# Kernel tuning notes

Hardware: AMD Instinct MI355X
Metric: run time of the kernel (lower is better)

The kernel has to match this reference:

```python
import jax, jax.numpy as jnp
import numpy as np

DIM = 512
HEADS = 8
HEAD_DIM = DIM // HEADS
SCALE = HEAD_DIM ** -0.5
EPS = 1e-5


def setup_inputs() -> dict:
    key = jax.random.key(0)
    ks = jax.random.split(key, 6)
    B, N, C = 4, 2048, DIM
    x = jax.random.normal(ks[0], (B, N, C), dtype=jnp.float32)
    w_qkv = jax.random.normal(ks[1], (C, 3 * C), dtype=jnp.float32) * (C ** -0.5)
    w_proj = jax.random.normal(ks[2], (C, C), dtype=jnp.float32) * (C ** -0.5)
    b_proj = jax.random.normal(ks[3], (C,), dtype=jnp.float32) * 0.02
    gamma = jnp.ones((C,), dtype=jnp.float32)
    beta = jnp.zeros((C,), dtype=jnp.float32)
    return {"x": x, "w_qkv": w_qkv, "w_proj": w_proj, "b_proj": b_proj,
            "gamma": gamma, "beta": beta}


def reference(x, w_qkv, w_proj, b_proj, gamma, beta):
    B, N, C = x.shape
    # LayerNorm over channel dim
    mu = jnp.mean(x, axis=-1, keepdims=True)
    var = jnp.mean(jnp.square(x - mu), axis=-1, keepdims=True)
    xn = (x - mu) * jax.lax.rsqrt(var + EPS) * gamma + beta
    # QKV projection (fp32, no bias)
    qkv = xn @ w_qkv  # [B, N, 3C]
    qkv = qkv.reshape(B, N, 3, HEADS, HEAD_DIM)
    q = jnp.transpose(qkv[:, :, 0], (0, 2, 1, 3))  # [B, H, N, D]
    k = jnp.transpose(qkv[:, :, 1], (0, 2, 1, 3))
    v = jnp.transpose(qkv[:, :, 2], (0, 2, 1, 3))
    attn = jnp.einsum('bhnd,bhmd->bhnm', q, k) * SCALE
    attn = jax.nn.softmax(attn, axis=-1)
    out = jnp.einsum('bhnm,bhmd->bhnd', attn, v)  # [B, H, N, D]
    out = jnp.transpose(out, (0, 2, 1, 3)).reshape(B, N, C)
    out = out @ w_proj + b_proj
    return x + out
```

## Files before the change

kernel.cpp:

```cpp
#include <hip/hip_runtime.h>
#include <hip/hip_bf16.h>
#include <math.h>

typedef _Float16 f16;
typedef _Float16 half8 __attribute__((ext_vector_type(8)));
typedef _Float16 half4 __attribute__((ext_vector_type(4)));
typedef float f32x4 __attribute__((ext_vector_type(4)));
typedef unsigned int uint;
typedef unsigned int u32x4 __attribute__((ext_vector_type(4)));

#define DIMC 512
#define HEADS 8
#define HD 64
#define BB 4
#define NN 2048
#define MM (BB*NN)
#define NQKV (3*DIMC)
#define SCALE 0.125f
#define LOG2E 1.44269504f
#define EPSLN 1e-5f

__device__ __forceinline__ void g2l16(const void* g, void* l) {
    __builtin_amdgcn_global_load_lds(
        (const __attribute__((address_space(1))) unsigned int*)g,
        (__attribute__((address_space(3))) unsigned int*)l, 16, 0, 0);
}

__device__ __forceinline__ void ln_rows(const float* __restrict__ x,
                                        const float* __restrict__ gamma,
                                        const float* __restrict__ beta,
                                        f16* __restrict__ xn, int blk) {
    int w = threadIdx.x >> 6;
    int lane = threadIdx.x & 63;
    int row = blk * 4 + w;
    const float* xr = x + (size_t)row * DIMC;
    float4 v0 = ((const float4*)xr)[lane * 2];
    float4 v1 = ((const float4*)xr)[lane * 2 + 1];
    float s = v0.x + v0.y + v0.z + v0.w + v1.x + v1.y + v1.z + v1.w;
#pragma unroll
    for (int off = 1; off < 64; off <<= 1) s += __shfl_xor(s, off);
    float mu = s * (1.0f / DIMC);
    float d0 = v0.x - mu, d1 = v0.y - mu, d2 = v0.z - mu, d3 = v0.w - mu;
    float d4 = v1.x - mu, d5 = v1.y - mu, d6 = v1.z - mu, d7 = v1.w - mu;
    float s2 = d0*d0 + d1*d1 + d2*d2 + d3*d3 + d4*d4 + d5*d5 + d6*d6 + d7*d7;
#pragma unroll
    for (int off = 1; off < 64; off <<= 1) s2 += __shfl_xor(s2, off);
    float rstd = rsqrtf(s2 * (1.0f / DIMC) + EPSLN);
    float4 g0 = ((const float4*)gamma)[lane * 2];
    float4 g1 = ((const float4*)gamma)[lane * 2 + 1];
    float4 b0 = ((const float4*)beta)[lane * 2];
    float4 b1 = ((const float4*)beta)[lane * 2 + 1];
    half8 o;
    o[0] = (f16)(d0 * rstd * g0.x + b0.x);
    o[1] = (f16)(d1 * rstd * g0.y + b0.y);
    o[2] = (f16)(d2 * rstd * g0.z + b0.z);
    o[3] = (f16)(d3 * rstd * g0.w + b0.w);
    o[4] = (f16)(d4 * rstd * g1.x + b1.x);
    o[5] = (f16)(d5 * rstd * g1.y + b1.y);
    o[6] = (f16)(d6 * rstd * g1.z + b1.z);
    o[7] = (f16)(d7 * rstd * g1.w + b1.w);
    ((half8*)(xn + (size_t)row * DIMC))[lane] = o;
}

__device__ __forceinline__ void transp_tile(const float* __restrict__ src,
                                            f16* __restrict__ dst,
                                            int R, int C, int k0, int n0) {
    __shared__ f16 t[32][72];
    int tid = threadIdx.x;
    int rr = tid >> 6, col = tid & 63;
#pragma unroll
    for (int p = 0; p < 8; p++) {
        int r = p * 4 + rr;
        t[r][col] = (f16)src[(size_t)(k0 + r) * C + n0 + col];
    }
    __syncthreads();
    int nl = tid >> 2, kc = (tid & 3) * 8;
    half8 v;
#pragma unroll
    for (int j = 0; j < 8; j++) v[j] = t[kc + j][nl];
    *(half8*)&dst[(size_t)(n0 + nl) * R + k0 + kc] = v;
}

__global__ __launch_bounds__(256) void prep_kernel(const float* __restrict__ x,
                                                   const float* __restrict__ gamma,
                                                   const float* __restrict__ beta,
                                                   const float* __restrict__ wqkv,
                                                   const float* __restrict__ wproj,
                                                   f16* __restrict__ xn,
                                                   f16* __restrict__ wqkvt,
                                                   f16* __restrict__ wprojt) {
    int bid = blockIdx.x;
    if (bid < 2048) {
        ln_rows(x, gamma, beta, xn, bid);
    } else if (bid < 2048 + 384) {
        int b2 = bid - 2048;
        int bx = b2 % 24, by = b2 / 24;
        transp_tile(wqkv, wqkvt, DIMC, NQKV, by * 32, bx * 64);
    } else {
        int b2 = bid - 2048 - 384;
        int bx = b2 % 8, by = b2 / 8;
        transp_tile(wproj, wprojt, DIMC, DIMC, by * 32, bx * 64);
    }
}

__device__ __forceinline__ void gemm128_loop(const char* Ag, const char* Bg,
                                             f16* As, f16* Bs, f32x4 (&acc)[4][4]) {
    int tid = threadIdx.x;
    int w = tid >> 6, lane = tid & 63, l15 = lane & 15, quad = lane >> 4;
    int wy = w >> 1, wx = w & 1;
    int off0 = w * 1024 + lane * 16;
    for (int kk = 0; kk < 16; ++kk) {
        __syncthreads();
#pragma unroll
        for (int c = 0; c < 2; ++c) {
            int off = c * 4096 + off0;
            int row = off >> 6, col = off & 63;
            g2l16(Ag + (size_t)row * 1024 + kk * 64 + col, (char*)As + c * 4096 + w * 1024);
            g2l16(Bg + (size_t)row * 1024 + kk * 64 + col, (char*)Bs + c * 4096 + w * 1024);
        }
        __syncthreads();
        half8 af[4], bf[4];
#pragma unroll
        for (int i = 0; i < 4; ++i) {
            af[i] = *(const half8*)((const char*)As + ((wy * 64 + i * 16 + l15) << 6) + quad * 16);
            bf[i] = *(const half8*)((const char*)Bs + ((wx * 64 + i * 16 + l15) << 6) + quad * 16);
        }
#pragma unroll
        for (int i = 0; i < 4; ++i)
#pragma unroll
            for (int j = 0; j < 4; ++j)
                acc[i][j] = __builtin_amdgcn_mfma_f32_16x16x32_f16(af[i], bf[j], acc[i][j], 0, 0, 0);
    }
}

__global__ __launch_bounds__(256) void gemm_qkv(const f16* __restrict__ xn,
                                                const f16* __restrict__ wt,
                                                f16* __restrict__ qb,
                                                f16* __restrict__ kbuf,
                                                f16* __restrict__ vtb) {
    __shared__ __align__(16) f16 As[128 * 32];
    __shared__ __align__(16) f16 Bs[128 * 32];
    int tid = threadIdx.x;
    int w = tid >> 6, lane = tid & 63, l15 = lane & 15, quad = lane >> 4;
    int wy = w >> 1, wx = w & 1;
    int m0 = blockIdx.y * 128, c0 = blockIdx.x * 128;
    f32x4 acc[4][4] = {};
    gemm128_loop((const char*)(xn + (size_t)m0 * DIMC),
                 (const char*)(wt + (size_t)c0 * DIMC), As, Bs, acc);
    int bx = blockIdx.x;
    if (bx < 8) {
        const float QS = SCALE * LOG2E;
        f16* dst = (bx < 4) ? qb : kbuf;
        float mul = (bx < 4) ? QS : 1.0f;
        int cb = (bx < 4) ? c0 : c0 - DIMC;
#pragma unroll
        for (int i = 0; i < 4; ++i)
#pragma unroll
            for (int j = 0; j < 4; ++j)
#pragma unroll
                for (int r = 0; r < 4; ++r) {
                    int m = m0 + wy * 64 + i * 16 + quad * 4 + r;
                    int c = cb + wx * 64 + j * 16 + l15;
                    int b = m >> 11, n = m & 2047;
                    int h = c >> 6, d = c & 63;
                    dst[(((size_t)(b * HEADS + h)) * NN + n) * HD + d] = (f16)(acc[i][j][r] * mul);
                }
    } else {
        __syncthreads();
        f16* T = (f16*)As + w * 512;
        int cb = c0 - 2 * DIMC;
        int dl = lane >> 2, mp = lane & 3;
#pragma unroll
        for (int i = 0; i < 4; ++i)
#pragma unroll
            for (int j = 0; j < 4; ++j) {
                half4 hv;
#pragma unroll
                for (int r = 0; r < 4; ++r) hv[r] = (f16)acc[i][j][r];
                *(half4*)&T[l15 * 20 + quad * 4] = hv;
                half4 rv = *(half4*)&T[dl * 20 + mp * 4];
                int c = cb + wx * 64 + j * 16 + dl;
                int m = m0 + wy * 64 + i * 16 + mp * 4;
                int b = m >> 11, n = m & 2047;
                int h = c >> 6, d = c & 63;
                *(half4*)&vtb[(((size_t)(b * HEADS + h)) * HD + d) * NN + n] = rv;
            }
    }
}

__global__ __launch_bounds__(256, 4) void attn_kernel(const f16* __restrict__ qb,
                                                      const f16* __restrict__ kbuf,
                                                      const f16* __restrict__ vtb,
                                                      f16* __restrict__ ao) {
    __shared__ __align__(16) f16 KV[8192];
    char* Kc = (char*)KV;
    char* Vc = (char*)(KV + 4096);
    int id = blockIdx.x;
    int xcd = id & 7, slot = id >> 3;
    int bh = xcd * 4 + (slot >> 4);
    int qt4 = slot & 15;
    int n0 = qt4 * 128;
    int tid = threadIdx.x, w = tid >> 6, lane = tid & 63, l15 = lane & 15, quad = lane >> 4;
    const f16* Kbase = kbuf + (size_t)bh * NN * HD;
    const f16* Vbase = vtb + (size_t)bh * HD * NN;
    const f16* Qbase = qb + (size_t)bh * NN * HD;
    half8 qf[2][2];
#pragma unroll
    for (int qt = 0; qt < 2; ++qt) {
        const f16* qr = Qbase + (size_t)(n0 + w * 32 + qt * 16 + l15) * HD + quad * 8;
        qf[qt][0] = *(const half8*)qr;
        qf[qt][1] = *(const half8*)(qr + 32);
    }
    f32x4 ot[2][4] = {};
    f32x4 lacc[2] = {};
    half8 ones8;
#pragma unroll
    for (int j = 0; j < 8; ++j) ones8[j] = (f16)1.0f;
    int srow = tid >> 2, part = (tid & 3) * 16;
    int sb = srow * 128, sx = (srow & 7) << 4;
    int scol = part * 2;
    int rx = (l15 & 7) << 4;
    half8 kp0, kp1, vp0, vp1;
    {
        const f16* kg = Kbase + (size_t)srow * HD + part;
        kp0 = ((const half8*)kg)[0]; kp1 = ((const half8*)kg)[1];
        const f16* vg = Vbase + (size_t)srow * NN + part;
        vp0 = ((const half8*)vg)[0]; vp1 = ((const half8*)vg)[1];
    }
    for (int it = 0; it < NN / 64; ++it) {
        __syncthreads();
        *(half8*)(Kc + sb + (scol ^ sx)) = kp0;
        *(half8*)(Kc + sb + ((scol + 16) ^ sx)) = kp1;
        *(half8*)(Vc + sb + (scol ^ sx)) = vp0;
        *(half8*)(Vc + sb + ((scol + 16) ^ sx)) = vp1;
        __syncthreads();
        if (it < NN / 64 - 1) {
            int kt0 = (it + 1) * 64;
            const f16* kg = Kbase + (size_t)(kt0 + srow) * HD + part;
            kp0 = ((const half8*)kg)[0]; kp1 = ((const half8*)kg)[1];
            const f16* vg = Vbase + (size_t)srow * NN + kt0 + part;
            vp0 = ((const half8*)vg)[0]; vp1 = ((const half8*)vg)[1];
        }
        f32x4 s0[4], s1[4];
        __builtin_amdgcn_s_setprio(1);
#pragma unroll
        for (int kt = 0; kt < 4; ++kt) {
            int rb = (kt * 16 + l15) * 128;
            half8 a0 = *(const half8*)(Kc + rb + ((quad * 16) ^ rx));
            half8 a1 = *(const half8*)(Kc + rb + ((64 + quad * 16) ^ rx));
            f32x4 z0 = {};
            z0 = __builtin_amdgcn_mfma_f32_16x16x32_f16(a0, qf[0][0], z0, 0, 0, 0);
            z0 = __builtin_amdgcn_mfma_f32_16x16x32_f16(a1, qf[0][1], z0, 0, 0, 0);
            s0[kt] = z0;
            f32x4 z1 = {};
            z1 = __builtin_amdgcn_mfma_f32_16x16x32_f16(a0, qf[1][0], z1, 0, 0, 0);
            z1 = __builtin_amdgcn_mfma_f32_16x16x32_f16(a1, qf[1][1], z1, 0, 0, 0);
            s1[kt] = z1;
        }
        __builtin_amdgcn_s_setprio(0);
        uint up[2][4][2];
#pragma unroll
        for (int kt = 0; kt < 4; ++kt) {
            up[0][kt][0] = __builtin_bit_cast(uint, __builtin_amdgcn_cvt_pkrtz(
                __builtin_amdgcn_exp2f(s0[kt][0]), __builtin_amdgcn_exp2f(s0[kt][1])));
            up[0][kt][1] = __builtin_bit_cast(uint, __builtin_amdgcn_cvt_pkrtz(
                __builtin_amdgcn_exp2f(s0[kt][2]), __builtin_amdgcn_exp2f(s0[kt][3])));
            up[1][kt][0] = __builtin_bit_cast(uint, __builtin_amdgcn_cvt_pkrtz(
                __builtin_amdgcn_exp2f(s1[kt][0]), __builtin_amdgcn_exp2f(s1[kt][1])));
            up[1][kt][1] = __builtin_bit_cast(uint, __builtin_amdgcn_cvt_pkrtz(
                __builtin_amdgcn_exp2f(s1[kt][2]), __builtin_amdgcn_exp2f(s1[kt][3])));
        }
        __builtin_amdgcn_s_setprio(1);
#pragma unroll
        for (int kc = 0; kc < 2; ++kc) {
            int cb = (kc * 64 + quad * 16) ^ rx;
            half8 av[4];
#pragma unroll
            for (int dt = 0; dt < 4; ++dt)
                av[dt] = *(const half8*)(Vc + (dt * 16 + l15) * 128 + cb);
#pragma unroll
            for (int qt = 0; qt < 2; ++qt) {
                u32x4 pw;
#pragma unroll
                for (int i = 0; i < 2; ++i) {
                    uint x = up[qt][kc * 2][i], y = up[qt][kc * 2 + 1][i];
                    asm volatile("v_permlane32_swap_b32 %0, %1" : "+v"(x), "+v"(y));
                    asm volatile("v_permlane16_swap_b32 %0, %1" : "+v"(x), "+v"(y));
                    pw[i] = x; pw[2 + i] = y;
                }
                half8 pb8 = __builtin_bit_cast(half8, pw);
                lacc[qt] = __builtin_amdgcn_mfma_f32_16x16x32_f16(ones8, pb8, lacc[qt], 0, 0, 0);
#pragma unroll
                for (int dt = 0; dt < 4; ++dt)
                    ot[qt][dt] = __builtin_amdgcn_mfma_f32_16x16x32_f16(av[dt], pb8, ot[qt][dt], 0, 0, 0);
            }
        }
        __builtin_amdgcn_s_setprio(0);
    }
    float inv[2] = { 1.0f / lacc[0][0], 1.0f / lacc[1][0] };
    __syncthreads();
    char* Tc = (char*)(KV + w * 2048);
#pragma unroll
    for (int qt = 0; qt < 2; ++qt)
#pragma unroll
        for (int dt = 0; dt < 4; ++dt) {
            half4 hv;
#pragma unroll
            for (int r = 0; r < 4; ++r) hv[r] = (f16)(ot[qt][dt][r] * inv[qt]);
            *(half4*)(Tc + (qt * 16 + l15) * 128 + ((dt * 32 + quad * 8) ^ rx)) = hv;
        }
    __syncthreads();
    int b = bh >> 3, h = bh & 7;
#pragma unroll
    for (int j = 0; j < 4; ++j) {
        int nl = j * 8 + (lane >> 3);
        int d16 = (lane & 7) * 16;
        half8 v = *(const half8*)(Tc + nl * 128 + (d16 ^ ((nl & 7) << 4)));
        int n = n0 + w * 32 + nl;
        *(half8*)&ao[((size_t)(b * NN + n)) * DIMC + h * HD + (lane & 7) * 8] = v;
    }
}

__global__ __launch_bounds__(256) void gemm_proj(const f16* __restrict__ aob,
                                                 const f16* __restrict__ wt,
                                                 const float* __restrict__ x,
                                                 const float* __restrict__ bias,
                                                 float* __restrict__ out) {
    __shared__ __align__(16) f16 As[128 * 32];
    __shared__ __align__(16) f16 Bs[64 * 32];
    int tid = threadIdx.x;
    int w = tid >> 6, lane = tid & 63, l15 = lane & 15, quad = lane >> 4;
    int m0 = blockIdx.y * 128, c0 = blockIdx.x * 64;
    const char* Ag = (const char*)(aob + (size_t)m0 * DIMC);
    const char* Bg = (const char*)(wt + (size_t)c0 * DIMC);
    f32x4 acc[2][4] = {};
    int off0 = w * 1024 + lane * 16;
    for (int kk = 0; kk < 16; ++kk) {
        __syncthreads();
#pragma unroll
        for (int c = 0; c < 2; ++c) {
            int off = c * 4096 + off0;
            int row = off >> 6, col = off & 63;
            g2l16(Ag + (size_t)row * 1024 + kk * 64 + col, (char*)As + c * 4096 + w * 1024);
        }
        {
            int off = tid * 16;
            int row = off >> 6, col = off & 63;
            g2l16(Bg + (size_t)row * 1024 + kk * 64 + col, (char*)Bs + w * 1024);
        }
        __syncthreads();
        half8 af[2], bf[4];
#pragma unroll
        for (int i = 0; i < 2; ++i)
            af[i] = *(const half8*)((const char*)As + ((w * 32 + i * 16 + l15) << 6) + quad * 16);
#pragma unroll
        for (int j = 0; j < 4; ++j)
            bf[j] = *(const half8*)((const char*)Bs + ((j * 16 + l15) << 6) + quad * 16);
#pragma unroll
        for (int i = 0; i < 2; ++i)
#pragma unroll
            for (int j = 0; j < 4; ++j)
                acc[i][j] = __builtin_amdgcn_mfma_f32_16x16x32_f16(af[i], bf[j], acc[i][j], 0, 0, 0);
    }
#pragma unroll
    for (int i = 0; i < 2; ++i)
#pragma unroll
        for (int j = 0; j < 4; ++j)
#pragma unroll
            for (int r = 0; r < 4; ++r) {
                int m = m0 + w * 32 + i * 16 + quad * 4 + r;
                int c = c0 + j * 16 + l15;
                out[(size_t)m * DIMC + c] = x[(size_t)m * DIMC + c] + bias[c] + acc[i][j][r];
            }
}

extern "C" void kernel_launch(void* const* d_in, const int* in_sizes, int n_in,
                              void* d_out, int out_size, void* d_ws, size_t ws_size,
                              hipStream_t stream) {
    (void)in_sizes; (void)n_in; (void)out_size; (void)ws_size;
    const float* x     = (const float*)d_in[0];
    const float* wqkv  = (const float*)d_in[1];
    const float* wproj = (const float*)d_in[2];
    const float* bproj = (const float*)d_in[3];
    const float* gamma = (const float*)d_in[4];
    const float* beta  = (const float*)d_in[5];
    float* out = (float*)d_out;

    char* ws = (char*)d_ws;
    f16* xn     = (f16*)ws;                 ws += (size_t)MM * DIMC * 2;
    f16* wqkvt  = (f16*)ws;                 ws += (size_t)NQKV * DIMC * 2;
    f16* wprojt = (f16*)ws;                 ws += (size_t)DIMC * DIMC * 2;
    f16* qbuf   = (f16*)ws;                 ws += (size_t)MM * DIMC * 2;
    f16* kbuf   = (f16*)ws;                 ws += (size_t)MM * DIMC * 2;
    f16* vtbuf  = (f16*)ws;                 ws += (size_t)MM * DIMC * 2;
    f16* aobuf  = (f16*)ws;                 ws += (size_t)MM * DIMC * 2;

    prep_kernel<<<2048 + 384 + 128, 256, 0, stream>>>(x, gamma, beta, wqkv, wproj,
                                                      xn, wqkvt, wprojt);
    gemm_qkv<<<dim3(NQKV / 128, MM / 128), 256, 0, stream>>>(xn, wqkvt, qbuf, kbuf, vtbuf);
    attn_kernel<<<NN / 128 * BB * HEADS, 256, 0, stream>>>(qbuf, kbuf, vtbuf, aobuf);
    gemm_proj<<<dim3(DIMC / 64, MM / 128), 256, 0, stream>>>(aobuf, wprojt, x, bproj, out);
}
```

Measured before the change: 156.5 us.

## Double-buffer 128-key K/V tiles in attention to halve barriers

The attention kernel now stages 128-key K/V tiles instead of 64-key ones. Shared memory is split into two 32 KB ping-pong buffers, which leaves one __syncthreads per iteration instead of two. The final barrier before the per-wave output transpose is also removed, since each wave reads back only its own shared-memory slice. In exchange, the kernel uses 64 KB of LDS and more prefetch registers, and launch bounds drop to 2 blocks per CU, which lowers occupancy.

```diff
diff --git a/kernel.cpp b/kernel.cpp
--- a/kernel.cpp
+++ b/kernel.cpp
@@ -188,13 +188,11 @@
     }
 }
 
-__global__ __launch_bounds__(256, 4) void attn_kernel(const f16* __restrict__ qb,
+__global__ __launch_bounds__(256, 2) void attn_kernel(const f16* __restrict__ qb,
                                                       const f16* __restrict__ kbuf,
                                                       const f16* __restrict__ vtb,
                                                       f16* __restrict__ ao) {
-    __shared__ __align__(16) f16 KV[8192];
-    char* Kc = (char*)KV;
-    char* Vc = (char*)(KV + 4096);
+    __shared__ __align__(16) char SMEM[65536];
     int id = blockIdx.x;
     int xcd = id & 7, slot = id >> 3;
     int bh = xcd * 4 + (slot >> 4);
@@ -216,90 +214,100 @@
     half8 ones8;
 #pragma unroll
     for (int j = 0; j < 8; ++j) ones8[j] = (f16)1.0f;
-    int srow = tid >> 2, part = (tid & 3) * 16;
-    int sb = srow * 128, sx = (srow & 7) << 4;
-    int scol = part * 2;
+    int kr = tid >> 1;
+    int kc0 = (tid & 1) * 64;
+    int ksw = (kr & 7) << 4;
+    int vd = tid >> 2;
+    int vc0 = (tid & 3) * 64;
+    int vsw = (vd & 7) << 4;
     int rx = (l15 & 7) << 4;
-    half8 kp0, kp1, vp0, vp1;
+    half8 kp[4], vp[4];
     {
-        const f16* kg = Kbase + (size_t)srow * HD + part;
-        kp0 = ((const half8*)kg)[0]; kp1 = ((const half8*)kg)[1];
-        const f16* vg = Vbase + (size_t)srow * NN + part;
-        vp0 = ((const half8*)vg)[0]; vp1 = ((const half8*)vg)[1];
-    }
-    for (int it = 0; it < NN / 64; ++it) {
-        __syncthreads();
-        *(half8*)(Kc + sb + (scol ^ sx)) = kp0;
-        *(half8*)(Kc + sb + ((scol + 16) ^ sx)) = kp1;
-        *(half8*)(Vc + sb + (scol ^ sx)) = vp0;
-        *(half8*)(Vc + sb + ((scol + 16) ^ sx)) = vp1;
-        __syncthreads();
-        if (it < NN / 64 - 1) {
-            int kt0 = (it + 1) * 64;
-            const f16* kg = Kbase + (size_t)(kt0 + srow) * HD + part;
-            kp0 = ((const half8*)kg)[0]; kp1 = ((const half8*)kg)[1];
-            const f16* vg = Vbase + (size_t)srow * NN + kt0 + part;
-            vp0 = ((const half8*)vg)[0]; vp1 = ((const half8*)vg)[1];
-        }
-        f32x4 s0[4], s1[4];
-        __builtin_amdgcn_s_setprio(1);
-#pragma unroll
-        for (int kt = 0; kt < 4; ++kt) {
-            int rb = (kt * 16 + l15) * 128;
-            half8 a0 = *(const half8*)(Kc + rb + ((quad * 16) ^ rx));
-            half8 a1 = *(const half8*)(Kc + rb + ((64 + quad * 16) ^ rx));
-            f32x4 z0 = {};
-            z0 = __builtin_amdgcn_mfma_f32_16x16x32_f16(a0, qf[0][0], z0, 0, 0, 0);
-            z0 = __builtin_amdgcn_mfma_f32_16x16x32_f16(a1, qf[0][1], z0, 0, 0, 0);
-            s0[kt] = z0;
-            f32x4 z1 = {};
-            z1 = __builtin_amdgcn_mfma_f32_16x16x32_f16(a0, qf[1][0], z1, 0, 0, 0);
-            z1 = __builtin_amdgcn_mfma_f32_16x16x32_f16(a1, qf[1][1], z1, 0, 0, 0);
-            s1[kt] = z1;
-        }
-        __builtin_amdgcn_s_setprio(0);
-        uint up[2][4][2];
-#pragma unroll
-        for (int kt = 0; kt < 4; ++kt) {
-            up[0][kt][0] = __builtin_bit_cast(uint, __builtin_amdgcn_cvt_pkrtz(
-                __builtin_amdgcn_exp2f(s0[kt][0]), __builtin_amdgcn_exp2f(s0[kt][1])));
-            up[0][kt][1] = __builtin_bit_cast(uint, __builtin_amdgcn_cvt_pkrtz(
-                __builtin_amdgcn_exp2f(s0[kt][2]), __builtin_amdgcn_exp2f(s0[kt][3])));
-            up[1][kt][0] = __builtin_bit_cast(uint, __builtin_amdgcn_cvt_pkrtz(
-                __builtin_amdgcn_exp2f(s1[kt][0]), __builtin_amdgcn_exp2f(s1[kt][1])));
-            up[1][kt][1] = __builtin_bit_cast(uint, __builtin_amdgcn_cvt_pkrtz(
-                __builtin_amdgcn_exp2f(s1[kt][2]), __builtin_amdgcn_exp2f(s1[kt][3])));
-        }
-        __builtin_amdgcn_s_setprio(1);
-#pragma unroll
-        for (int kc = 0; kc < 2; ++kc) {
-            int cb = (kc * 64 + quad * 16) ^ rx;
-            half8 av[4];
-#pragma unroll
-            for (int dt = 0; dt < 4; ++dt)
-                av[dt] = *(const half8*)(Vc + (dt * 16 + l15) * 128 + cb);
-#pragma unroll
-            for (int qt = 0; qt < 2; ++qt) {
-                u32x4 pw;
-#pragma unroll
-                for (int i = 0; i < 2; ++i) {
-                    uint x = up[qt][kc * 2][i], y = up[qt][kc * 2 + 1][i];
-                    asm volatile("v_permlane32_swap_b32 %0, %1" : "+v"(x), "+v"(y));
-                    asm volatile("v_permlane16_swap_b32 %0, %1" : "+v"(x), "+v"(y));
-                    pw[i] = x; pw[2 + i] = y;
+        const half8* kg = (const half8*)(Kbase + (size_t)kr * HD + (tid & 1) * 32);
+        kp[0] = kg[0]; kp[1] = kg[1]; kp[2] = kg[2]; kp[3] = kg[3];
+        const half8* vg = (const half8*)(Vbase + (size_t)vd * NN + (tid & 3) * 32);
+        vp[0] = vg[0]; vp[1] = vg[1]; vp[2] = vg[2]; vp[3] = vg[3];
+    }
+    for (int it = 0; it < NN / 128; ++it) {
+        int bo = (it & 1) << 14;
+        char* Kc = SMEM + bo;
+        char* Vc = SMEM + 32768 + bo;
+#pragma unroll
+        for (int j = 0; j < 4; ++j)
+            *(half8*)(Kc + kr * 128 + ((kc0 + j * 16) ^ ksw)) = kp[j];
+#pragma unroll
+        for (int j = 0; j < 4; ++j)
+            *(half8*)(Vc + vd * 256 + ((vc0 + j * 16) ^ vsw)) = vp[j];
+        __syncthreads();
+        if (it < NN / 128 - 1) {
+            int k0 = (it + 1) * 128;
+            const half8* kg = (const half8*)(Kbase + (size_t)(k0 + kr) * HD + (tid & 1) * 32);
+            kp[0] = kg[0]; kp[1] = kg[1]; kp[2] = kg[2]; kp[3] = kg[3];
+            const half8* vg = (const half8*)(Vbase + (size_t)vd * NN + k0 + (tid & 3) * 32);
+            vp[0] = vg[0]; vp[1] = vg[1]; vp[2] = vg[2]; vp[3] = vg[3];
+        }
+#pragma unroll
+        for (int h = 0; h < 2; ++h) {
+            f32x4 s0[4], s1[4];
+            __builtin_amdgcn_s_setprio(1);
+#pragma unroll
+            for (int i = 0; i < 4; ++i) {
+                int rb = ((h * 4 + i) * 16 + l15) * 128;
+                half8 a0 = *(const half8*)(Kc + rb + ((quad * 16) ^ rx));
+                half8 a1 = *(const half8*)(Kc + rb + ((64 + quad * 16) ^ rx));
+                f32x4 z0 = {};
+                z0 = __builtin_amdgcn_mfma_f32_16x16x32_f16(a0, qf[0][0], z0, 0, 0, 0);
+                z0 = __builtin_amdgcn_mfma_f32_16x16x32_f16(a1, qf[0][1], z0, 0, 0, 0);
+                s0[i] = z0;
+                f32x4 z1 = {};
+                z1 = __builtin_amdgcn_mfma_f32_16x16x32_f16(a0, qf[1][0], z1, 0, 0, 0);
+                z1 = __builtin_amdgcn_mfma_f32_16x16x32_f16(a1, qf[1][1], z1, 0, 0, 0);
+                s1[i] = z1;
+            }
+            __builtin_amdgcn_s_setprio(0);
+            uint up[2][4][2];
+#pragma unroll
+            for (int i = 0; i < 4; ++i) {
+                up[0][i][0] = __builtin_bit_cast(uint, __builtin_amdgcn_cvt_pkrtz(
+                    __builtin_amdgcn_exp2f(s0[i][0]), __builtin_amdgcn_exp2f(s0[i][1])));
+                up[0][i][1] = __builtin_bit_cast(uint, __builtin_amdgcn_cvt_pkrtz(
+                    __builtin_amdgcn_exp2f(s0[i][2]), __builtin_amdgcn_exp2f(s0[i][3])));
+                up[1][i][0] = __builtin_bit_cast(uint, __builtin_amdgcn_cvt_pkrtz(
+                    __builtin_amdgcn_exp2f(s1[i][0]), __builtin_amdgcn_exp2f(s1[i][1])));
+                up[1][i][1] = __builtin_bit_cast(uint, __builtin_amdgcn_cvt_pkrtz(
+                    __builtin_amdgcn_exp2f(s1[i][2]), __builtin_amdgcn_exp2f(s1[i][3])));
+            }
+            __builtin_amdgcn_s_setprio(1);
+#pragma unroll
+            for (int j = 0; j < 2; ++j) {
+                int cb = (((h * 2 + j) * 64) + quad * 16) ^ rx;
+                half8 av[4];
+#pragma unroll
+                for (int dt = 0; dt < 4; ++dt)
+                    av[dt] = *(const half8*)(Vc + (dt * 16 + l15) * 256 + cb);
+#pragma unroll
+                for (int qt = 0; qt < 2; ++qt) {
+                    u32x4 pw;
+#pragma unroll
+                    for (int i = 0; i < 2; ++i) {
+                        uint x = up[qt][j * 2][i], y = up[qt][j * 2 + 1][i];
+                        asm volatile("v_permlane32_swap_b32 %0, %1" : "+v"(x), "+v"(y));
+                        asm volatile("v_permlane16_swap_b32 %0, %1" : "+v"(x), "+v"(y));
+                        pw[i] = x; pw[2 + i] = y;
+                    }
+                    half8 pb8 = __builtin_bit_cast(half8, pw);
+                    lacc[qt] = __builtin_amdgcn_mfma_f32_16x16x32_f16(ones8, pb8, lacc[qt], 0, 0, 0);
+#pragma unroll
+                    for (int dt = 0; dt < 4; ++dt)
+                        ot[qt][dt] = __builtin_amdgcn_mfma_f32_16x16x32_f16(av[dt], pb8, ot[qt][dt], 0, 0, 0);
                 }
-                half8 pb8 = __builtin_bit_cast(half8, pw);
-                lacc[qt] = __builtin_amdgcn_mfma_f32_16x16x32_f16(ones8, pb8, lacc[qt], 0, 0, 0);
-#pragma unroll
-                for (int dt = 0; dt < 4; ++dt)
-                    ot[qt][dt] = __builtin_amdgcn_mfma_f32_16x16x32_f16(av[dt], pb8, ot[qt][dt], 0, 0, 0);
             }
-        }
-        __builtin_amdgcn_s_setprio(0);
+            __builtin_amdgcn_s_setprio(0);
+        }
     }
     float inv[2] = { 1.0f / lacc[0][0], 1.0f / lacc[1][0] };
     __syncthreads();
-    char* Tc = (char*)(KV + w * 2048);
+    char* Tc = SMEM + w * 4096;
 #pragma unroll
     for (int qt = 0; qt < 2; ++qt)
 #pragma unroll
@@ -309,15 +317,14 @@
             for (int r = 0; r < 4; ++r) hv[r] = (f16)(ot[qt][dt][r] * inv[qt]);
             *(half4*)(Tc + (qt * 16 + l15) * 128 + ((dt * 32 + quad * 8) ^ rx)) = hv;
         }
-    __syncthreads();
-    int b = bh >> 3, h = bh & 7;
+    int b = bh >> 3, h2 = bh & 7;
 #pragma unroll
     for (int j = 0; j < 4; ++j) {
         int nl = j * 8 + (lane >> 3);
         int d16 = (lane & 7) * 16;
         half8 v = *(const half8*)(Tc + nl * 128 + (d16 ^ ((nl & 7) << 4)));
         int n = n0 + w * 32 + nl;
-        *(half8*)&ao[((size_t)(b * NN + n)) * DIMC + h * HD + (lane & 7) * 8] = v;
+        *(half8*)&ao[((size_t)(b * NN + n)) * DIMC + h2 * HD + (lane & 7) * 8] = v;
     }
 }
 
```

New measurement: 158.3 us. Within noise of the previous version (+1.2%).

## Double-buffer LDS tiles in QKV and projection GEMM main loops

Applied to the files above, without the earlier changes.

Both GEMM kernels now keep two LDS stages. Each iteration issues async global-to-LDS loads for the next k-tile before running MFMAs on the current one, and uses one barrier per iteration instead of two. The goal is to hide global load latency behind matrix math. The cost is double the shared memory per block, which may lower occupancy. There is also a correctness concern: the barrier may not wait for the async global_load_lds to complete (vmcnt) before the next iteration reads the buffer.

```diff
diff --git a/kernel.cpp b/kernel.cpp
--- a/kernel.cpp
+++ b/kernel.cpp
@@ -109,28 +109,33 @@
     int w = tid >> 6, lane = tid & 63, l15 = lane & 15, quad = lane >> 4;
     int wy = w >> 1, wx = w & 1;
     int off0 = w * 1024 + lane * 16;
+#define QSTAGE(kk, b) do { \
+    _Pragma("unroll") \
+    for (int c = 0; c < 2; ++c) { \
+        int off = c * 4096 + off0; \
+        int row = off >> 6, col = off & 63; \
+        g2l16(Ag + (size_t)row * 1024 + (kk) * 64 + col, (char*)As + (b) * 8192 + c * 4096 + w * 1024); \
+        g2l16(Bg + (size_t)row * 1024 + (kk) * 64 + col, (char*)Bs + (b) * 8192 + c * 4096 + w * 1024); \
+    } } while (0)
+    QSTAGE(0, 0);
+    __syncthreads();
     for (int kk = 0; kk < 16; ++kk) {
-        __syncthreads();
-#pragma unroll
-        for (int c = 0; c < 2; ++c) {
-            int off = c * 4096 + off0;
-            int row = off >> 6, col = off & 63;
-            g2l16(Ag + (size_t)row * 1024 + kk * 64 + col, (char*)As + c * 4096 + w * 1024);
-            g2l16(Bg + (size_t)row * 1024 + kk * 64 + col, (char*)Bs + c * 4096 + w * 1024);
-        }
-        __syncthreads();
+        int cb = kk & 1;
+        if (kk < 15) QSTAGE(kk + 1, cb ^ 1);
         half8 af[4], bf[4];
 #pragma unroll
         for (int i = 0; i < 4; ++i) {
-            af[i] = *(const half8*)((const char*)As + ((wy * 64 + i * 16 + l15) << 6) + quad * 16);
-            bf[i] = *(const half8*)((const char*)Bs + ((wx * 64 + i * 16 + l15) << 6) + quad * 16);
+            af[i] = *(const half8*)((const char*)As + cb * 8192 + ((wy * 64 + i * 16 + l15) << 6) + quad * 16);
+            bf[i] = *(const half8*)((const char*)Bs + cb * 8192 + ((wx * 64 + i * 16 + l15) << 6) + quad * 16);
         }
 #pragma unroll
         for (int i = 0; i < 4; ++i)
 #pragma unroll
             for (int j = 0; j < 4; ++j)
                 acc[i][j] = __builtin_amdgcn_mfma_f32_16x16x32_f16(af[i], bf[j], acc[i][j], 0, 0, 0);
-    }
+        __syncthreads();
+    }
+#undef QSTAGE
 }
 
 __global__ __launch_bounds__(256) void gemm_qkv(const f16* __restrict__ xn,
@@ -138,8 +143,8 @@
                                                 f16* __restrict__ qb,
                                                 f16* __restrict__ kbuf,
                                                 f16* __restrict__ vtb) {
-    __shared__ __align__(16) f16 As[128 * 32];
-    __shared__ __align__(16) f16 Bs[128 * 32];
+    __shared__ __align__(16) f16 As[2 * 128 * 32];
+    __shared__ __align__(16) f16 Bs[2 * 128 * 32];
     int tid = threadIdx.x;
     int w = tid >> 6, lane = tid & 63, l15 = lane & 15, quad = lane >> 4;
     int wy = w >> 1, wx = w & 1;
@@ -326,8 +331,8 @@
                                                  const float* __restrict__ x,
                                                  const float* __restrict__ bias,
                                                  float* __restrict__ out) {
-    __shared__ __align__(16) f16 As[128 * 32];
-    __shared__ __align__(16) f16 Bs[64 * 32];
+    __shared__ __align__(16) f16 As[2 * 128 * 32];
+    __shared__ __align__(16) f16 Bs[2 * 64 * 32];
     int tid = threadIdx.x;
     int w = tid >> 6, lane = tid & 63, l15 = lane & 15, quad = lane >> 4;
     int m0 = blockIdx.y * 128, c0 = blockIdx.x * 64;
@@ -335,33 +340,38 @@
     const char* Bg = (const char*)(wt + (size_t)c0 * DIMC);
     f32x4 acc[2][4] = {};
     int off0 = w * 1024 + lane * 16;
+#define PSTAGE(kk, b) do { \
+    _Pragma("unroll") \
+    for (int c = 0; c < 2; ++c) { \
+        int off = c * 4096 + off0; \
+        int row = off >> 6, col = off & 63; \
+        g2l16(Ag + (size_t)row * 1024 + (kk) * 64 + col, (char*)As + (b) * 8192 + c * 4096 + w * 1024); \
+    } \
+    { \
+        int off = tid * 16; \
+        int row = off >> 6, col = off & 63; \
+        g2l16(Bg + (size_t)row * 1024 + (kk) * 64 + col, (char*)Bs + (b) * 4096 + w * 1024); \
+    } } while (0)
+    PSTAGE(0, 0);
+    __syncthreads();
     for (int kk = 0; kk < 16; ++kk) {
-        __syncthreads();
-#pragma unroll
-        for (int c = 0; c < 2; ++c) {
-            int off = c * 4096 + off0;
-            int row = off >> 6, col = off & 63;
-            g2l16(Ag + (size_t)row * 1024 + kk * 64 + col, (char*)As + c * 4096 + w * 1024);
-        }
-        {
-            int off = tid * 16;
-            int row = off >> 6, col = off & 63;
-            g2l16(Bg + (size_t)row * 1024 + kk * 64 + col, (char*)Bs + w * 1024);
-        }
-        __syncthreads();
+        int cb = kk & 1;
+        if (kk < 15) PSTAGE(kk + 1, cb ^ 1);
         half8 af[2], bf[4];
 #pragma unroll
         for (int i = 0; i < 2; ++i)
-            af[i] = *(const half8*)((const char*)As + ((w * 32 + i * 16 + l15) << 6) + quad * 16);
+            af[i] = *(const half8*)((const char*)As + cb * 8192 + ((w * 32 + i * 16 + l15) << 6) + quad * 16);
 #pragma unroll
         for (int j = 0; j < 4; ++j)
-            bf[j] = *(const half8*)((const char*)Bs + ((j * 16 + l15) << 6) + quad * 16);
+            bf[j] = *(const half8*)((const char*)Bs + cb * 4096 + ((j * 16 + l15) << 6) + quad * 16);
 #pragma unroll
         for (int i = 0; i < 2; ++i)
 #pragma unroll
             for (int j = 0; j < 4; ++j)
                 acc[i][j] = __builtin_amdgcn_mfma_f32_16x16x32_f16(af[i], bf[j], acc[i][j], 0, 0, 0);
-    }
+        __syncthreads();
+    }
+#undef PSTAGE
 #pragma unroll
     for (int i = 0; i < 2; ++i)
 #pragma unroll
```

Measured after the change: 157.4 us. Within noise of the previous version (+0.6%).
